# Performance work log

Hardware: AMD Instinct MI355X
Metric: run time of the kernel (lower is better)

Reference implementation:

```python
import jax, jax.numpy as jnp
import numpy as np

H = 16  # num heads

def setup_inputs() -> dict:
    key = jax.random.key(0)
    ks = jax.random.split(key, 5)
    B, T, E = 4, 2048, 1024
    return {
        "x": jax.random.normal(ks[0], (B, T, E), dtype=jnp.float32),
        "in_proj_weight": jax.random.normal(ks[1], (3 * E, E), dtype=jnp.float32) * (1.0 / np.sqrt(E)),
        "in_proj_bias": jax.random.normal(ks[2], (3 * E,), dtype=jnp.float32) * 0.02,
        "out_w": jax.random.normal(ks[3], (E, E), dtype=jnp.float32) * (1.0 / np.sqrt(E)),
        "out_b": jax.random.normal(ks[4], (E,), dtype=jnp.float32) * 0.02,
    }


def reference(x, in_proj_weight, in_proj_bias, out_w, out_b):
    B, T, E = x.shape
    D = E // H
    scale = D ** -0.5
    wq, wk, wv = jnp.split(in_proj_weight, 3, axis=0)  # each [E, E]
    bq, bk, bv = jnp.split(in_proj_bias, 3, axis=0)
    # projections (self-attention: q=k=v source)
    q = (x @ wq.T + bq) * scale            # [B, T, E]
    k = x @ wk.T + bk
    v = x @ wv.T + bv
    # split heads -> [B, H, T, D]
    def heads(t):
        return t.reshape(B, T, H, D).transpose(0, 2, 1, 3)
    q, k, v = heads(q), heads(k), heads(v)
    scores = jnp.einsum('bhqd,bhkd->bhqk', q, k)       # [B, H, T, T]
    probs = jax.nn.softmax(scores, axis=-1)
    attn = jnp.einsum('bhqk,bhkd->bhqd', probs, v)     # [B, H, T, D]
    attn = attn.transpose(0, 2, 1, 3).reshape(B, T, E)
    out = attn @ out_w.T + out_b                       # out_proj (nn.Linear)
    return (out, probs / scale)
```

## Files before the change

kernel.cpp:

```cpp
#include <hip/hip_runtime.h>


#define DEV __device__ __forceinline__

typedef __attribute__((ext_vector_type(8))) short short8;
typedef __attribute__((ext_vector_type(4))) float f32x4;

DEV unsigned short f2b(float f) {
  union { float f; unsigned u; } v; v.f = f;
  unsigned r = v.u + 0x7fffu + ((v.u >> 16) & 1u);
  return (unsigned short)(r >> 16);
}
DEV unsigned pk2(float lo, float hi) {
  return (unsigned)f2b(lo) | ((unsigned)f2b(hi) << 16);
}
#if __has_builtin(__builtin_amdgcn_exp2f)
DEV float exp2_fast(float x) { return __builtin_amdgcn_exp2f(x); }
#else
DEV float exp2_fast(float x) { return exp2f(x); }
#endif
DEV void gl_lds16(const void* g, void* l) {
  __builtin_amdgcn_global_load_lds(
      (const __attribute__((address_space(1))) void*)g,
      (__attribute__((address_space(3))) void*)l, 16, 0, 0);
}
DEV void bar_lgkm() { asm volatile("s_waitcnt lgkmcnt(0)\n\ts_barrier" ::: "memory"); }

__global__ void cvt_f32_bf16(const float* __restrict__ src, unsigned short* __restrict__ dst, int n) {
  int i = (blockIdx.x * blockDim.x + threadIdx.x) * 4;
  if (i >= n) return;
  float4 v = *(const float4*)(src + i);
  ushort4 o; o.x = f2b(v.x); o.y = f2b(v.y); o.z = f2b(v.z); o.w = f2b(v.w);
  *(ushort4*)(dst + i) = o;
}

template<int MODE>
__global__ __launch_bounds__(256, 2) void gemm_bt(
    const unsigned short* __restrict__ A,
    const unsigned short* __restrict__ B,
    const float* __restrict__ bias,
    float* __restrict__ Cf,
    unsigned short* __restrict__ Cqk,
    unsigned short* __restrict__ Vtg,
    int N, int K)
{
  constexpr int BK = 64;
  __shared__ __align__(16) unsigned short As[128*BK];
  __shared__ __align__(16) unsigned short Bs[128*BK];
  const int tid = threadIdx.x, lane = tid & 63, wid = tid >> 6;
  const int lhi = lane >> 4, llo = lane & 15;
  const int m0 = blockIdx.y * 128, n0 = blockIdx.x * 128;
  const int wr = wid >> 1, wc = wid & 1;

  f32x4 acc[4][4] = {};

  const int nsteps = K / BK;
  for (int kt = 0; kt < nsteps; ++kt) {
    __syncthreads();
#pragma unroll
    for (int s = 0; s < 4; ++s) {
      int u = wid*4 + s;
      int a = u*1024 + lane*16;
      int t = a >> 7;
      int cb = (a & 127) ^ ((t & 7) << 4);
      int e = kt*BK + (cb >> 1);
      gl_lds16(A + (size_t)(m0 + t)*K + e, (char*)As + u*1024);
      gl_lds16(B + (size_t)(n0 + t)*K + e, (char*)Bs + u*1024);
    }
    __syncthreads();
#pragma unroll
    for (int kk = 0; kk < 2; ++kk) {
      short8 af[4], bfr[4];
#pragma unroll
      for (int mf = 0; mf < 4; ++mf) {
        int row = wr*64 + mf*16 + llo;
        af[mf] = *(const short8*)((const char*)As + row*128 + ((kk*64 + lhi*16) ^ ((row & 7) << 4)));
      }
#pragma unroll
      for (int nf = 0; nf < 4; ++nf) {
        int row = wc*64 + nf*16 + llo;
        bfr[nf] = *(const short8*)((const char*)Bs + row*128 + ((kk*64 + lhi*16) ^ ((row & 7) << 4)));
      }
#pragma unroll
      for (int mf = 0; mf < 4; ++mf)
#pragma unroll
        for (int nf = 0; nf < 4; ++nf)
          acc[mf][nf] = __builtin_amdgcn_mfma_f32_16x16x32_bf16(af[mf], bfr[nf], acc[mf][nf], 0, 0, 0);
    }
  }
  if (MODE == 0) {
#pragma unroll
    for (int mf = 0; mf < 4; ++mf)
#pragma unroll
      for (int nf = 0; nf < 4; ++nf) {
        int n = n0 + wc*64 + nf*16 + llo;
        float bv = bias[n];
#pragma unroll
        for (int r = 0; r < 4; ++r) {
          int m = m0 + wr*64 + mf*16 + lhi*4 + r;
          __builtin_nontemporal_store(acc[mf][nf][r] + bv, &Cf[(size_t)m*N + n]);
        }
      }
  } else {
    if (n0 < 2048) {
#pragma unroll
      for (int mf = 0; mf < 4; ++mf)
#pragma unroll
        for (int nf = 0; nf < 4; ++nf) {
          int n = n0 + wc*64 + nf*16 + llo;
          float bv = bias[n];
          float sc = (n < 1024) ? 0.125f * 1.44269504088896f : 1.0f;
#pragma unroll
          for (int r = 0; r < 4; ++r) {
            int m = m0 + wr*64 + mf*16 + lhi*4 + r;
            Cqk[(size_t)m*2048 + n] = f2b((acc[mf][nf][r] + bv) * sc);
          }
        }
    } else {
#pragma unroll
      for (int mf = 0; mf < 4; ++mf)
#pragma unroll
        for (int nf = 0; nf < 4; ++nf) {
          int n = n0 + wc*64 + nf*16 + llo;
          float bv = bias[n];
          int hh = (n - 2048) >> 6, d = (n - 2048) & 63;
          int m = m0 + wr*64 + mf*16 + lhi*4;
          int bb = m >> 11, t = m & 2047;
          ushort4 o;
          o.x = f2b(acc[mf][nf][0] + bv);
          o.y = f2b(acc[mf][nf][1] + bv);
          o.z = f2b(acc[mf][nf][2] + bv);
          o.w = f2b(acc[mf][nf][3] + bv);
          *(ushort4*)(Vtg + ((size_t)((bb << 4) + hh)*64 + d)*2048 + t) = o;
        }
    }
  }
}

__global__ __launch_bounds__(256, 2) void mha_fused(
    const unsigned short* __restrict__ qk,
    const unsigned short* __restrict__ vtg,
    float* __restrict__ probs,
    unsigned short* __restrict__ attnb)
{
  constexpr int T = 2048, LD = 2048, QB = 64, TB = 128, NT = T / TB;
  __shared__ __align__(16) unsigned short Qs[QB*64];
  __shared__ __align__(16) unsigned short Kbuf[2][TB*64];
  __shared__ __align__(16) unsigned short Vs[64*TB];
  __shared__ __align__(16) unsigned short Ps[QB*TB];
  __shared__ float lsum[4][QB];
  __shared__ float linv[QB];

  const int tid = threadIdx.x, lane = tid & 63, wid = tid >> 6;
  const int lhi = lane >> 4, llo = lane & 15;
  const int wg = ((blockIdx.x & 7) << 8) | (blockIdx.x >> 3);
  const int qt = wg & 31, bh = wg >> 5;
  const int bb = bh >> 4, h = bh & 15;
  const int q0 = qt * QB;
  const size_t tokQ = (size_t)bb*T + q0;

  auto stageK = [&](int tt, unsigned short* buf) {
#pragma unroll
    for (int s = 0; s < 4; ++s) {
      int u = wid*4 + s;
      int a = u*1024 + lane*16;
      int tr = a >> 7;
      int cb = (a & 127) ^ ((tr & 7) << 4);
      gl_lds16(qk + ((size_t)bb*T + tt*TB + tr)*LD + 1024 + h*64 + (cb >> 1),
               (char*)buf + u*1024);
    }
  };
  auto stageV = [&](int tt) {
#pragma unroll
    for (int s = 0; s < 4; ++s) {
      int u = wid*4 + s;
      int a = u*1024 + lane*16;
      int d = a >> 8;
      int cb = (a & 255) ^ ((d & 7) << 4);
      gl_lds16(vtg + ((size_t)bh*64 + d)*T + tt*TB + (cb >> 1),
               (char*)Vs + u*1024);
    }
  };

#pragma unroll
  for (int s = 0; s < 2; ++s) {
    int u = wid*2 + s;
    int a = u*1024 + lane*16;
    int tr = a >> 7;
    int cb = (a & 127) ^ ((tr & 7) << 4);
    gl_lds16(qk + (tokQ + tr)*LD + h*64 + (cb >> 1), (char*)Qs + u*1024);
  }
  stageK(0, Kbuf[0]);
  asm volatile("s_waitcnt vmcnt(4)" ::: "memory");
  __builtin_amdgcn_s_barrier();

  short8 qfr[4][2];
#pragma unroll
  for (int qf = 0; qf < 4; ++qf)
#pragma unroll
    for (int kk = 0; kk < 2; ++kk) {
      int row = qf*16 + llo;
      qfr[qf][kk] = *(const short8*)((const char*)Qs + row*128 + ((kk*64 + lhi*16) ^ ((row & 7) << 4)));
    }

  float part[4] = {0.f, 0.f, 0.f, 0.f};
  for (int tt = 0; tt < NT; ++tt) {
    stageK((tt + 1) & 15, Kbuf[(tt + 1) & 1]);
    asm volatile("s_waitcnt vmcnt(4)" ::: "memory");
    f32x4 sacc[2][4] = {};
#pragma unroll
    for (int kk = 0; kk < 2; ++kk) {
      short8 kf[2];
#pragma unroll
      for (int tf = 0; tf < 2; ++tf) {
        int row = wid*32 + tf*16 + llo;
        kf[tf] = *(const short8*)((const char*)Kbuf[tt & 1] + row*128 + ((kk*64 + lhi*16) ^ ((row & 7) << 4)));
      }
#pragma unroll
      for (int tf = 0; tf < 2; ++tf)
#pragma unroll
        for (int qf = 0; qf < 4; ++qf)
          sacc[tf][qf] = __builtin_amdgcn_mfma_f32_16x16x32_bf16(kf[tf], qfr[qf][kk], sacc[tf][qf], 0, 0, 0);
    }
#pragma unroll
    for (int tf = 0; tf < 2; ++tf)
#pragma unroll
      for (int qf = 0; qf < 4; ++qf)
#pragma unroll
        for (int r = 0; r < 4; ++r)
          part[qf] += exp2_fast(sacc[tf][qf][r]);
  }

#pragma unroll
  for (int qf = 0; qf < 4; ++qf) {
    float v = part[qf];
    v += __shfl_xor(v, 16);
    v += __shfl_xor(v, 32);
    if (lhi == 0) lsum[wid][qf*16 + llo] = v;
  }
  bar_lgkm();
  if (tid < QB) linv[tid] = 1.0f / (lsum[0][tid] + lsum[1][tid] + lsum[2][tid] + lsum[3][tid]);
  stageV(0);
  stageK(1, Kbuf[1]);
  asm volatile("s_waitcnt vmcnt(8)" ::: "memory");
  bar_lgkm();
  float lr[4];
#pragma unroll
  for (int qf = 0; qf < 4; ++qf) lr[qf] = linv[qf*16 + llo];

  f32x4 pv[4] = {};
  for (int tt = 0; tt < NT; ++tt) {
    f32x4 sacc[2][4] = {};
#pragma unroll
    for (int kk = 0; kk < 2; ++kk) {
      short8 kf[2];
#pragma unroll
      for (int tf = 0; tf < 2; ++tf) {
        int row = wid*32 + tf*16 + llo;
        kf[tf] = *(const short8*)((const char*)Kbuf[tt & 1] + row*128 + ((kk*64 + lhi*16) ^ ((row & 7) << 4)));
      }
#pragma unroll
      for (int tf = 0; tf < 2; ++tf)
#pragma unroll
        for (int qf = 0; qf < 4; ++qf)
          sacc[tf][qf] = __builtin_amdgcn_mfma_f32_16x16x32_bf16(kf[tf], qfr[qf][kk], sacc[tf][qf], 0, 0, 0);
    }
    f32x4 pst[2][4];
#pragma unroll
    for (int tf = 0; tf < 2; ++tf)
#pragma unroll
      for (int qf = 0; qf < 4; ++qf) {
        float p0 = exp2_fast(sacc[tf][qf][0]) * lr[qf];
        float p1 = exp2_fast(sacc[tf][qf][1]) * lr[qf];
        float p2 = exp2_fast(sacc[tf][qf][2]) * lr[qf];
        float p3 = exp2_fast(sacc[tf][qf][3]) * lr[qf];
        int q = qf*16 + llo;
        int t0 = wid*32 + tf*16 + lhi*4;
        uint2 w2; w2.x = pk2(p0, p1); w2.y = pk2(p2, p3);
        *(uint2*)((char*)Ps + q*256 + ((t0*2) ^ ((q & 7) << 4))) = w2;
        f32x4 pv4; pv4[0] = 8.f*p0; pv4[1] = 8.f*p1; pv4[2] = 8.f*p2; pv4[3] = 8.f*p3;
        pst[tf][qf] = pv4;
      }
    if (tt == 0) asm volatile("s_waitcnt vmcnt(4) lgkmcnt(0)\n\ts_barrier" ::: "memory");
    else         asm volatile("s_waitcnt vmcnt(12) lgkmcnt(0)\n\ts_barrier" ::: "memory");
#pragma unroll
    for (int kk2 = 0; kk2 < 4; ++kk2) {
      int rq = wid*16 + llo;
      short8 pb = *(const short8*)((const char*)Ps + rq*256 + ((kk2*64 + lhi*16) ^ ((rq & 7) << 4)));
#pragma unroll
      for (int mf = 0; mf < 4; ++mf) {
        int rd = mf*16 + llo;
        short8 va = *(const short8*)((const char*)Vs + rd*256 + ((kk2*64 + lhi*16) ^ ((rd & 7) << 4)));
        pv[mf] = __builtin_amdgcn_mfma_f32_16x16x32_bf16(va, pb, pv[mf], 0, 0, 0);
      }
    }
    if (tt == 0) asm volatile("s_waitcnt vmcnt(0)\n\ts_barrier" ::: "memory");
    else         asm volatile("s_waitcnt vmcnt(8)\n\ts_barrier" ::: "memory");
    stageV((tt + 1) & 15);
    asm volatile("" ::: "memory");
    stageK((tt + 2) & 15, Kbuf[tt & 1]);
    asm volatile("" ::: "memory");
#pragma unroll
    for (int tf = 0; tf < 2; ++tf)
#pragma unroll
      for (int qf = 0; qf < 4; ++qf) {
        int q = qf*16 + llo;
        int t0 = wid*32 + tf*16 + lhi*4;
        f32x4* dst = (f32x4*)&probs[((size_t)bh*T + q0 + q)*T + tt*TB + t0];
        __builtin_nontemporal_store(pst[tf][qf], dst);
      }
  }

#pragma unroll
  for (int mf = 0; mf < 4; ++mf) {
    int q = wid*16 + llo;
    int d0 = mf*16 + lhi*4;
    ushort4 o;
    o.x = f2b(pv[mf][0]); o.y = f2b(pv[mf][1]);
    o.z = f2b(pv[mf][2]); o.w = f2b(pv[mf][3]);
    *(ushort4*)(attnb + (tokQ + q)*1024 + h*64 + d0) = o;
  }
}

extern "C" void kernel_launch(void* const* d_in, const int* in_sizes, int n_in,
                              void* d_out, int out_size, void* d_ws, size_t ws_size,
                              hipStream_t stream) {
  (void)in_sizes; (void)n_in; (void)out_size; (void)ws_size;
  const float* x    = (const float*)d_in[0];
  const float* wqkv = (const float*)d_in[1];
  const float* bqkv = (const float*)d_in[2];
  const float* wout = (const float*)d_in[3];
  const float* bout = (const float*)d_in[4];

  constexpr int T = 2048, E = 1024;
  constexpr int M = 4 * T;
  constexpr size_t NX   = (size_t)M * E;
  constexpr size_t NW1  = (size_t)3 * E * E;
  constexpr size_t NW2  = (size_t)E * E;
  constexpr size_t NQK  = (size_t)M * 2048;
  constexpr size_t NVT  = (size_t)64 * 64 * T;

  char* ws = (char*)d_ws;
  unsigned short* xb    = (unsigned short*)ws;  ws += NX  * 2;
  unsigned short* wqkvb = (unsigned short*)ws;  ws += NW1 * 2;
  unsigned short* woutb = (unsigned short*)ws;  ws += NW2 * 2;
  unsigned short* qkb   = (unsigned short*)ws;  ws += NQK * 2;
  unsigned short* vtg   = (unsigned short*)ws;  ws += NVT * 2;
  unsigned short* attnb = (unsigned short*)ws;  ws += NX  * 2;

  cvt_f32_bf16<<<(int)(NX  / 1024), 256, 0, stream>>>(x,    xb,    (int)NX);
  cvt_f32_bf16<<<(int)(NW1 / 1024), 256, 0, stream>>>(wqkv, wqkvb, (int)NW1);
  cvt_f32_bf16<<<(int)(NW2 / 1024), 256, 0, stream>>>(wout, woutb, (int)NW2);

  gemm_bt<1><<<dim3(3*E/128, M/128), 256, 0, stream>>>(
      xb, wqkvb, bqkv, nullptr, qkb, vtg, 3*E, E);

  float* probsOut = (float*)d_out + NX;
  mha_fused<<<4*16*(T/64), 256, 0, stream>>>(qkb, vtg, probsOut, attnb);

  gemm_bt<0><<<dim3(E/128, M/128), 256, 0, stream>>>(
      attnb, woutb, bout, (float*)d_out, nullptr, nullptr, E, E);
}
```

Baseline: 419.8 us.

## Shrink LDS footprint of fused attention to fit three blocks per CU

```diff
diff --git a/kernel.cpp b/kernel.cpp
--- a/kernel.cpp
+++ b/kernel.cpp
@@ -137,16 +137,15 @@
   }
 }
 
-__global__ __launch_bounds__(256, 2) void mha_fused(
+__global__ __launch_bounds__(256, 3) void mha_fused(
     const unsigned short* __restrict__ qk,
     const unsigned short* __restrict__ vtg,
     float* __restrict__ probs,
     unsigned short* __restrict__ attnb)
 {
   constexpr int T = 2048, LD = 2048, QB = 64, TB = 128, NT = T / TB;
-  __shared__ __align__(16) unsigned short Qs[QB*64];
-  __shared__ __align__(16) unsigned short Kbuf[2][TB*64];
-  __shared__ __align__(16) unsigned short Vs[64*TB];
+  __shared__ __align__(16) unsigned short Kslot[TB*64];
+  __shared__ __align__(16) unsigned short Vslot[64*TB];
   __shared__ __align__(16) unsigned short Ps[QB*TB];
   __shared__ float lsum[4][QB];
   __shared__ float linv[QB];
@@ -178,7 +177,7 @@
       int d = a >> 8;
       int cb = (a & 255) ^ ((d & 7) << 4);
       gl_lds16(vtg + ((size_t)bh*64 + d)*T + tt*TB + (cb >> 1),
-               (char*)Vs + u*1024);
+               (char*)Vslot + u*1024);
     }
   };
 
@@ -188,9 +187,9 @@
     int a = u*1024 + lane*16;
     int tr = a >> 7;
     int cb = (a & 127) ^ ((tr & 7) << 4);
-    gl_lds16(qk + (tokQ + tr)*LD + h*64 + (cb >> 1), (char*)Qs + u*1024);
-  }
-  stageK(0, Kbuf[0]);
+    gl_lds16(qk + (tokQ + tr)*LD + h*64 + (cb >> 1), (char*)Ps + u*1024);
+  }
+  stageK(0, Kslot);
   asm volatile("s_waitcnt vmcnt(4)" ::: "memory");
   __builtin_amdgcn_s_barrier();
 
@@ -200,13 +199,15 @@
 #pragma unroll
     for (int kk = 0; kk < 2; ++kk) {
       int row = qf*16 + llo;
-      qfr[qf][kk] = *(const short8*)((const char*)Qs + row*128 + ((kk*64 + lhi*16) ^ ((row & 7) << 4)));
+      qfr[qf][kk] = *(const short8*)((const char*)Ps + row*128 + ((kk*64 + lhi*16) ^ ((row & 7) << 4)));
     }
 
   float part[4] = {0.f, 0.f, 0.f, 0.f};
   for (int tt = 0; tt < NT; ++tt) {
-    stageK((tt + 1) & 15, Kbuf[(tt + 1) & 1]);
+    unsigned short* nxt = ((tt + 1) & 1) ? Vslot : Kslot;
+    stageK((tt + 1) & 15, nxt);
     asm volatile("s_waitcnt vmcnt(4)" ::: "memory");
+    const unsigned short* cur = (tt & 1) ? Vslot : Kslot;
     f32x4 sacc[2][4] = {};
 #pragma unroll
     for (int kk = 0; kk < 2; ++kk) {
@@ -214,7 +215,7 @@
 #pragma unroll
       for (int tf = 0; tf < 2; ++tf) {
         int row = wid*32 + tf*16 + llo;
-        kf[tf] = *(const short8*)((const char*)Kbuf[tt & 1] + row*128 + ((kk*64 + lhi*16) ^ ((row & 7) << 4)));
+        kf[tf] = *(const short8*)((const char*)cur + row*128 + ((kk*64 + lhi*16) ^ ((row & 7) << 4)));
       }
 #pragma unroll
       for (int tf = 0; tf < 2; ++tf)
@@ -241,8 +242,6 @@
   bar_lgkm();
   if (tid < QB) linv[tid] = 1.0f / (lsum[0][tid] + lsum[1][tid] + lsum[2][tid] + lsum[3][tid]);
   stageV(0);
-  stageK(1, Kbuf[1]);
-  asm volatile("s_waitcnt vmcnt(8)" ::: "memory");
   bar_lgkm();
   float lr[4];
 #pragma unroll
@@ -250,6 +249,8 @@
 
   f32x4 pv[4] = {};
   for (int tt = 0; tt < NT; ++tt) {
+    if (tt == 0) asm volatile("s_waitcnt vmcnt(4)"  ::: "memory");
+    else         asm volatile("s_waitcnt vmcnt(12)" ::: "memory");
     f32x4 sacc[2][4] = {};
 #pragma unroll
     for (int kk = 0; kk < 2; ++kk) {
@@ -257,7 +258,7 @@
 #pragma unroll
       for (int tf = 0; tf < 2; ++tf) {
         int row = wid*32 + tf*16 + llo;
-        kf[tf] = *(const short8*)((const char*)Kbuf[tt & 1] + row*128 + ((kk*64 + lhi*16) ^ ((row & 7) << 4)));
+        kf[tf] = *(const short8*)((const char*)Kslot + row*128 + ((kk*64 + lhi*16) ^ ((row & 7) << 4)));
       }
 #pragma unroll
       for (int tf = 0; tf < 2; ++tf)
@@ -265,7 +266,9 @@
         for (int qf = 0; qf < 4; ++qf)
           sacc[tf][qf] = __builtin_amdgcn_mfma_f32_16x16x32_bf16(kf[tf], qfr[qf][kk], sacc[tf][qf], 0, 0, 0);
     }
-    f32x4 pst[2][4];
+    asm volatile("s_waitcnt lgkmcnt(0)" ::: "memory");
+    __builtin_amdgcn_sched_barrier(0);
+    stageK((tt + 1) & 15, Kslot);
 #pragma unroll
     for (int tf = 0; tf < 2; ++tf)
 #pragma unroll
@@ -279,10 +282,10 @@
         uint2 w2; w2.x = pk2(p0, p1); w2.y = pk2(p2, p3);
         *(uint2*)((char*)Ps + q*256 + ((t0*2) ^ ((q & 7) << 4))) = w2;
         f32x4 pv4; pv4[0] = 8.f*p0; pv4[1] = 8.f*p1; pv4[2] = 8.f*p2; pv4[3] = 8.f*p3;
-        pst[tf][qf] = pv4;
-      }
-    if (tt == 0) asm volatile("s_waitcnt vmcnt(4) lgkmcnt(0)\n\ts_barrier" ::: "memory");
-    else         asm volatile("s_waitcnt vmcnt(12) lgkmcnt(0)\n\ts_barrier" ::: "memory");
+        __builtin_nontemporal_store(pv4,
+            (f32x4*)&probs[((size_t)bh*T + q0 + q)*T + tt*TB + t0]);
+      }
+    asm volatile("s_waitcnt vmcnt(12) lgkmcnt(0)\n\ts_barrier" ::: "memory");
 #pragma unroll
     for (int kk2 = 0; kk2 < 4; ++kk2) {
       int rq = wid*16 + llo;
@@ -290,25 +293,12 @@
 #pragma unroll
       for (int mf = 0; mf < 4; ++mf) {
         int rd = mf*16 + llo;
-        short8 va = *(const short8*)((const char*)Vs + rd*256 + ((kk2*64 + lhi*16) ^ ((rd & 7) << 4)));
+        short8 va = *(const short8*)((const char*)Vslot + rd*256 + ((kk2*64 + lhi*16) ^ ((rd & 7) << 4)));
         pv[mf] = __builtin_amdgcn_mfma_f32_16x16x32_bf16(va, pb, pv[mf], 0, 0, 0);
       }
     }
-    if (tt == 0) asm volatile("s_waitcnt vmcnt(0)\n\ts_barrier" ::: "memory");
-    else         asm volatile("s_waitcnt vmcnt(8)\n\ts_barrier" ::: "memory");
+    asm volatile("s_waitcnt lgkmcnt(0)\n\ts_barrier" ::: "memory");
     stageV((tt + 1) & 15);
-    asm volatile("" ::: "memory");
-    stageK((tt + 2) & 15, Kbuf[tt & 1]);
-    asm volatile("" ::: "memory");
-#pragma unroll
-    for (int tf = 0; tf < 2; ++tf)
-#pragma unroll
-      for (int qf = 0; qf < 4; ++qf) {
-        int q = qf*16 + llo;
-        int t0 = wid*32 + tf*16 + lhi*4;
-        f32x4* dst = (f32x4*)&probs[((size_t)bh*T + q0 + q)*T + tt*TB + t0];
-        __builtin_nontemporal_store(pst[tf][qf], dst);
-      }
   }
 
 #pragma unroll
```

Result: faster. 372.1 us (-11.4%).
